# Kernel tuning notes

Hardware: AMD Instinct MI355X
Metric: run time of the kernel (lower is better)

Reference implementation:

```python
import jax, jax.numpy as jnp
import numpy as np

D = 4096
N = 8192


def fwht(x):
    """Fast Walsh-Hadamard Transform (orthonormal, divided by sqrt(d)).

    log2(d) butterfly stages, each a single vectorized add/sub over the
    full tensor. Loop bound is static (log2 of trailing dim), jit-safe.
    """
    d = x.shape[-1]
    leading = x.shape[:-1]
    h = 1
    while h < d:
        x = x.reshape(*leading, d // (2 * h), 2, h)
        a = x[..., 0, :]
        b = x[..., 1, :]
        x = jnp.stack([a + b, a - b], axis=-2).reshape(*leading, d)
        h *= 2
    return x * jnp.asarray(d, x.dtype) ** -0.5


def setup_inputs() -> dict:
    key = jax.random.key(0)
    kx, ks = jax.random.split(key)
    x = jax.random.normal(kx, (N, D), dtype=jnp.float32)
    # deterministic random +/-1 sign vector (buffer of RHTRotation)
    signs = (jax.random.randint(ks, (D,), 0, 2).astype(jnp.float32) * 2.0 - 1.0)
    return {"x": x, "signs": signs}


def reference(x, signs):
    # randomized_hadamard: y = H @ (D x) / sqrt(d), D = diag(signs)
    return fwht(x * signs)
```

## Files before the change

kernel.cpp:

```cpp
#include <hip/hip_runtime.h>

#define D 4096

__global__ __launch_bounds__(256, 4) void fwht_kernel(const float* __restrict__ x,
                                                      const float* __restrict__ signs,
                                                      float* __restrict__ out,
                                                      int rows) {
    const int lane = threadIdx.x & 63;
    const int wid = threadIdx.x >> 6;
    const long row = (long)blockIdx.x * 4 + wid;
    if (row >= rows) return;

    const float4* __restrict__ xv = (const float4*)(x + row * (long)D);
    const float4* __restrict__ sv = (const float4*)signs;
    float4* __restrict__ ov = (float4*)(out + row * (long)D);

    float v[64];

#pragma unroll
    for (int k = 0; k < 16; k++) {
        float4 a = xv[k * 64 + lane];
        float4 s = sv[k * 64 + lane];
        v[4 * k + 0] = a.x * s.x;
        v[4 * k + 1] = a.y * s.y;
        v[4 * k + 2] = a.z * s.z;
        v[4 * k + 3] = a.w * s.w;
    }

#pragma unroll
    for (int k = 0; k < 16; k++) {
        float a0 = v[4 * k + 0], a1 = v[4 * k + 1];
        float a2 = v[4 * k + 2], a3 = v[4 * k + 3];
        float b0 = a0 + a1, b1 = a0 - a1;
        float b2 = a2 + a3, b3 = a2 - a3;
        v[4 * k + 0] = b0 + b2;
        v[4 * k + 1] = b1 + b3;
        v[4 * k + 2] = b0 - b2;
        v[4 * k + 3] = b1 - b3;
    }

#pragma unroll
    for (int s = 1; s < 64; s <<= 1) {
        const float sgn = (lane & s) ? -1.0f : 1.0f;
#pragma unroll
        for (int i = 0; i < 64; i++) {
            float p = __shfl_xor(v[i], s, 64);
            v[i] = fmaf(sgn, v[i], p);
        }
    }

#pragma unroll
    for (int s = 1; s < 16; s <<= 1) {
#pragma unroll
        for (int k = 0; k < 16; k++) {
            if (!(k & s)) {
#pragma unroll
                for (int j = 0; j < 4; j++) {
                    float a = v[4 * k + j];
                    float b = v[4 * (k ^ s) + j];
                    v[4 * k + j] = a + b;
                    v[4 * (k ^ s) + j] = a - b;
                }
            }
        }
    }

    const float scale = 1.0f / 64.0f;
#pragma unroll
    for (int k = 0; k < 16; k++) {
        float4 r;
        r.x = v[4 * k + 0] * scale;
        r.y = v[4 * k + 1] * scale;
        r.z = v[4 * k + 2] * scale;
        r.w = v[4 * k + 3] * scale;
        ov[k * 64 + lane] = r;
    }
}

extern "C" void kernel_launch(void* const* d_in, const int* in_sizes, int n_in,
                              void* d_out, int out_size, void* d_ws, size_t ws_size,
                              hipStream_t stream) {
    const float* x = (const float*)d_in[0];
    const float* signs = (const float*)d_in[1];
    float* out = (float*)d_out;
    const int rows = in_sizes[0] / D;
    const int blocks = (rows + 3) / 4;
    fwht_kernel<<<dim3(blocks), dim3(256), 0, stream>>>(x, signs, out, rows);
}
```

Measured before the change: 244.6 us.

## Replace cross-lane shuffle butterflies with register FWHT plus swizzled LDS transpose

Each row now runs as a single-wave block. The kernel does a 64-point Walsh-Hadamard transform fully in registers, transposes through XOR-swizzled shared memory, then does a second 64-point register transform. This replaces the 384 per-thread cross-lane shuffles of the old butterfly stages with a few LDS reads and writes, and the swizzle is meant to avoid bank conflicts. In exchange each block uses 16 KB of LDS and holds only one wave, which may limit occupancy and latency hiding. The row-bounds guard is also dropped, which assumes the row count is exact.

```diff
diff --git a/kernel.cpp b/kernel.cpp
--- a/kernel.cpp
+++ b/kernel.cpp
@@ -2,14 +2,28 @@
 
 #define D 4096
 
-__global__ __launch_bounds__(256, 4) void fwht_kernel(const float* __restrict__ x,
-                                                      const float* __restrict__ signs,
-                                                      float* __restrict__ out,
-                                                      int rows) {
-    const int lane = threadIdx.x & 63;
-    const int wid = threadIdx.x >> 6;
-    const long row = (long)blockIdx.x * 4 + wid;
-    if (row >= rows) return;
+__device__ __forceinline__ void fwht64_reg(float v[64]) {
+#pragma unroll
+    for (int s = 1; s < 64; s <<= 1) {
+#pragma unroll
+        for (int i = 0; i < 64; i++) {
+            if (!(i & s)) {
+                float a = v[i], b = v[i ^ s];
+                v[i]     = a + b;
+                v[i ^ s] = a - b;
+            }
+        }
+    }
+}
+
+__global__ __launch_bounds__(64, 2) void fwht_kernel(const float* __restrict__ x,
+                                                     const float* __restrict__ signs,
+                                                     float* __restrict__ out) {
+    __shared__ float lds[D];
+    char* const ldsb = (char*)lds;
+
+    const int lane = threadIdx.x;
+    const long row = blockIdx.x;
 
     const float4* __restrict__ xv = (const float4*)(x + row * (long)D);
     const float4* __restrict__ sv = (const float4*)signs;
@@ -27,52 +41,39 @@
         v[4 * k + 3] = a.w * s.w;
     }
 
+    fwht64_reg(v);
+
+    const int lo4 = (lane & 15) << 4;
+    const int hi2 = (lane & 48) << 4;
 #pragma unroll
     for (int k = 0; k < 16; k++) {
-        float a0 = v[4 * k + 0], a1 = v[4 * k + 1];
-        float a2 = v[4 * k + 2], a3 = v[4 * k + 3];
-        float b0 = a0 + a1, b1 = a0 - a1;
-        float b2 = a2 + a3, b3 = a2 - a3;
-        v[4 * k + 0] = b0 + b2;
-        v[4 * k + 1] = b1 + b3;
-        v[4 * k + 2] = b0 - b2;
-        v[4 * k + 3] = b1 - b3;
+        const int addr = (k << 10) + ((lo4 ^ (k << 4)) + hi2);
+        *(float4*)(ldsb + addr) =
+            make_float4(v[4 * k + 0], v[4 * k + 1], v[4 * k + 2], v[4 * k + 3]);
     }
 
+    const int kk = lane >> 2, jj = lane & 3;
+    const int rbase = (kk << 10) + (jj << 2);
+    const int kx = kk << 4;
 #pragma unroll
-    for (int s = 1; s < 64; s <<= 1) {
-        const float sgn = (lane & s) ? -1.0f : 1.0f;
-#pragma unroll
-        for (int i = 0; i < 64; i++) {
-            float p = __shfl_xor(v[i], s, 64);
-            v[i] = fmaf(sgn, v[i], p);
-        }
-    }
+    for (int l = 0; l < 64; l++)
+        v[l] = *(const float*)(ldsb + rbase + (((l << 4) ^ kx)));
+
+    fwht64_reg(v);
 
 #pragma unroll
-    for (int s = 1; s < 16; s <<= 1) {
-#pragma unroll
-        for (int k = 0; k < 16; k++) {
-            if (!(k & s)) {
-#pragma unroll
-                for (int j = 0; j < 4; j++) {
-                    float a = v[4 * k + j];
-                    float b = v[4 * (k ^ s) + j];
-                    v[4 * k + j] = a + b;
-                    v[4 * (k ^ s) + j] = a - b;
-                }
-            }
-        }
-    }
+    for (int l = 0; l < 64; l++)
+        *(float*)(ldsb + rbase + (((l << 4) ^ kx))) = v[l];
 
     const float scale = 1.0f / 64.0f;
 #pragma unroll
     for (int k = 0; k < 16; k++) {
-        float4 r;
-        r.x = v[4 * k + 0] * scale;
-        r.y = v[4 * k + 1] * scale;
-        r.z = v[4 * k + 2] * scale;
-        r.w = v[4 * k + 3] * scale;
+        const int addr = (k << 10) + ((lo4 ^ (k << 4)) + hi2);
+        float4 r = *(const float4*)(ldsb + addr);
+        r.x *= scale;
+        r.y *= scale;
+        r.z *= scale;
+        r.w *= scale;
         ov[k * 64 + lane] = r;
     }
 }
@@ -84,6 +85,5 @@
     const float* signs = (const float*)d_in[1];
     float* out = (float*)d_out;
     const int rows = in_sizes[0] / D;
-    const int blocks = (rows + 3) / 4;
-    fwht_kernel<<<dim3(blocks), dim3(256), 0, stream>>>(x, signs, out, rows);
+    fwht_kernel<<<dim3(rows), dim3(64), 0, stream>>>(x, signs, out);
 }
```

New measurement: 229.5 us. 6.2% less time.
